# Performance work log

Measured on AMD Instinct MI355X. Metric: run time of the kernel, lower is better.

Reference implementation:

```python
import jax, jax.numpy as jnp
import numpy as np

N_NODES = 50000
N_EDGES = 800000
IN_F = 128
HID_F = 128
OUT_F = 128
BATCH = 2


def setup_inputs() -> dict:
    key = jax.random.key(0)
    ks = jax.random.split(key, 12)
    inputs = jax.random.normal(ks[0], (BATCH, N_NODES, IN_F), dtype=jnp.float32)
    src = jax.random.randint(ks[1], (N_EDGES,), 0, N_NODES, dtype=jnp.int32)
    dst = jax.random.randint(ks[2], (N_EDGES,), 0, N_NODES, dtype=jnp.int32)
    s = 0.05
    return {
        "inputs": inputs, "src": src, "dst": dst,
        "W_self1": jax.random.normal(ks[3], (HID_F, IN_F), jnp.float32) * s,
        "W_neigh1": jax.random.normal(ks[4], (HID_F, IN_F), jnp.float32) * s,
        "b1": jnp.zeros((HID_F,), jnp.float32),
        "W_self2": jax.random.normal(ks[5], (HID_F, HID_F), jnp.float32) * s,
        "W_neigh2": jax.random.normal(ks[6], (HID_F, HID_F), jnp.float32) * s,
        "b2": jnp.zeros((HID_F,), jnp.float32),
        "W_self3": jax.random.normal(ks[7], (OUT_F, HID_F), jnp.float32) * s,
        "W_neigh3": jax.random.normal(ks[8], (OUT_F, HID_F), jnp.float32) * s,
        "b3": jnp.zeros((OUT_F,), jnp.float32),
    }


def _sage_layer(h, src, dst, deg_inv, W_self, W_neigh, b):
    # h: [N, d]; mean-aggregate over in-neighbors (src -> dst)
    msg = h[src]                                              # [E, d] gather
    agg = jax.ops.segment_sum(msg, dst, num_segments=N_NODES)  # [N, d]
    agg = agg * deg_inv[:, None]                               # mean (0 for deg-0 nodes, DGL convention)
    out = h @ W_self.T + agg @ W_neigh.T + b
    # SAGEConv activation=ReLU; outer F.relu after conv1/conv2 is idempotent
    return jax.nn.relu(out)


def reference(inputs, src, dst, W_self1, W_neigh1, b1, W_self2, W_neigh2, b2, W_self3, W_neigh3, b3):
    deg = jax.ops.segment_sum(jnp.ones((N_EDGES,), jnp.float32), dst, num_segments=N_NODES)
    deg_inv = jnp.where(deg > 0, 1.0 / jnp.maximum(deg, 1.0), 0.0)

    def per_graph(x):  # x: [N, in_feats]
        h = _sage_layer(x, src, dst, deg_inv, W_self1, W_neigh1, b1)
        h = _sage_layer(h, src, dst, deg_inv, W_self2, W_neigh2, b2)
        h = _sage_layer(h, src, dst, deg_inv, W_self3, W_neigh3, b3)
        return h

    return jax.vmap(per_graph)(inputs)  # [B, N, out_feats]
```

## Files before the change

### kernel.cpp

```cpp
#include <hip/hip_runtime.h>

#define NN 50000
#define NE 800000
#define F  128
#define NB 2
#define M2 (NB * NN)

typedef __attribute__((ext_vector_type(8))) short     bf16x8;
typedef __attribute__((ext_vector_type(4))) float     f32x4;
typedef __attribute__((ext_vector_type(8))) unsigned short u16x8;
typedef __attribute__((ext_vector_type(4))) unsigned short u16x4;

__device__ inline unsigned short f2bf_rn(float f) {
    unsigned u = __float_as_uint(f);
    u += 0x7FFFu + ((u >> 16) & 1u);
    return (unsigned short)(u >> 16);
}
__device__ inline float bf2f(unsigned short h) {
    return __uint_as_float(((unsigned)h) << 16);
}


__global__ void count_kernel(const int* __restrict__ dst, int* __restrict__ cnt) {
    int e = blockIdx.x * blockDim.x + threadIdx.x;
    if (e < NE) atomicAdd(&cnt[dst[e]], 1);
}

__global__ __launch_bounds__(1024) void scan1_kernel(const int* __restrict__ cnt,
                                                     int* __restrict__ local_ex,
                                                     int* __restrict__ blocksums) {
    __shared__ int sd[1024];
    int i = blockIdx.x * 1024 + threadIdx.x;
    int v = (i < NN) ? cnt[i] : 0;
    sd[threadIdx.x] = v;
    __syncthreads();
    for (int off = 1; off < 1024; off <<= 1) {
        int t = 0;
        if ((int)threadIdx.x >= off) t = sd[threadIdx.x - off];
        __syncthreads();
        sd[threadIdx.x] += t;
        __syncthreads();
    }
    if (i < NN) local_ex[i] = sd[threadIdx.x] - v;
    if (threadIdx.x == 1023) blocksums[blockIdx.x] = sd[1023];
}

__global__ void scan2_kernel(int* __restrict__ bs, int nb) {
    int lane = threadIdx.x;
    int v = (lane < nb) ? bs[lane] : 0;
    for (int off = 1; off < 64; off <<= 1) {
        int t = __shfl_up(v, off);
        if (lane >= off) v += t;
    }
    int ex = __shfl_up(v, 1);
    if (lane == 0) ex = 0;
    if (lane < nb) bs[lane] = ex;
}

__global__ void scan3_kernel(const int* __restrict__ local_ex, const int* __restrict__ bs,
                             const int* __restrict__ cnt,
                             int* __restrict__ rowptr, float* __restrict__ dinv) {
    int i = blockIdx.x * blockDim.x + threadIdx.x;
    if (i < NN) {
        rowptr[i] = local_ex[i] + bs[i >> 10];
        int d = cnt[i];
        dinv[i] = (d > 0) ? 1.0f / (float)d : 0.0f;
    }
    if (i == 0) rowptr[NN] = NE;
}

__global__ void fill_kernel(const int* __restrict__ src, const int* __restrict__ dst,
                            const int* __restrict__ rowptr, int* __restrict__ cursor,
                            unsigned short* __restrict__ eidx) {
    int e = blockIdx.x * blockDim.x + threadIdx.x;
    if (e < NE) {
        int d = dst[e];
        int p = rowptr[d] + atomicAdd(&cursor[d], 1);
        eidx[p] = (unsigned short)src[e];
    }
}


__global__ void wsplit_kernel(const float* __restrict__ Ws0, const float* __restrict__ Wn0,
                              const float* __restrict__ Ws1, const float* __restrict__ Wn1,
                              const float* __restrict__ Ws2, const float* __restrict__ Wn2,
                              unsigned short* __restrict__ hi, unsigned short* __restrict__ lo) {
    int idx = blockIdx.x * blockDim.x + threadIdx.x;
    int l = idx >> 15;
    int r = idx & 32767;
    int j = r >> 8, k = r & 255;
    const float* Ws = (l == 0) ? Ws0 : (l == 1) ? Ws1 : Ws2;
    const float* Wn = (l == 0) ? Wn0 : (l == 1) ? Wn1 : Wn2;
    float v = (k < 128) ? Ws[j * 128 + k] : Wn[j * 128 + (k - 128)];
    unsigned short h = f2bf_rn(v);
    hi[idx] = h;
    lo[idx] = f2bf_rn(v - bf2f(h));
}


__global__ void xsplit_kernel(const float* __restrict__ x,
                              unsigned short* __restrict__ hi, unsigned short* __restrict__ lo) {
    size_t idx = (size_t)blockIdx.x * blockDim.x + threadIdx.x;
    float4 v = *reinterpret_cast<const float4*>(&x[idx * 4]);
    int f4 = (int)(idx & 31);
    size_t row = idx >> 5;
    int b = (row >= NN) ? 1 : 0;
    size_t n = row - (size_t)b * NN;
    size_t o = ((n << 1) + b) * F + f4 * 4;
    u16x4 h4, l4;
    float vv[4] = {v.x, v.y, v.z, v.w};
#pragma unroll
    for (int i = 0; i < 4; ++i) {
        unsigned short h = f2bf_rn(vv[i]);
        h4[i] = h;
        l4[i] = f2bf_rn(vv[i] - bf2f(h));
    }
    *reinterpret_cast<u16x4*>(&hi[o]) = h4;
    *reinterpret_cast<u16x4*>(&lo[o]) = l4;
}


__global__ void aggregate_bf16(const unsigned short* __restrict__ h,
                               const int* __restrict__ rowptr, const unsigned short* __restrict__ eidx,
                               const float* __restrict__ dinv,
                               unsigned short* __restrict__ agg_hi, unsigned short* __restrict__ agg_lo) {
    int gtid = blockIdx.x * blockDim.x + threadIdx.x;
    int node = gtid >> 6;
    int lane = gtid & 63;
    if (node >= NN) return;
    int g = lane >> 5, li = lane & 31;
    int s0 = rowptr[node], s1 = rowptr[node + 1];

    float acc[8] = {0.f, 0.f, 0.f, 0.f, 0.f, 0.f, 0.f, 0.f};

    for (int e = s0; e < s1; e += 8) {
        int sidx[4];
        u16x8 vv[4];
#pragma unroll
        for (int j = 0; j < 4; ++j) {
            int ee = e + 2 * j + g;
            sidx[j] = (ee < s1) ? (int)eidx[ee] : -1;
        }
#pragma unroll
        for (int j = 0; j < 4; ++j)
            if (sidx[j] >= 0)
                vv[j] = *reinterpret_cast<const u16x8*>(&h[(size_t)sidx[j] * 256 + li * 8]);
#pragma unroll
        for (int j = 0; j < 4; ++j)
            if (sidx[j] >= 0) {
#pragma unroll
                for (int i = 0; i < 8; ++i) acc[i] += bf2f(vv[j][i]);
            }
    }

#pragma unroll
    for (int i = 0; i < 8; ++i) acc[i] += __shfl_xor(acc[i], 32);

    if (g == 0) {
        float di = dinv[node];
        u16x8 h8, l8;
#pragma unroll
        for (int i = 0; i < 8; ++i) {
            float v = acc[i] * di;
            unsigned short hh = f2bf_rn(v);
            h8[i] = hh;
            l8[i] = f2bf_rn(v - bf2f(hh));
        }
        *reinterpret_cast<u16x8*>(&agg_hi[(size_t)node * 256 + li * 8]) = h8;
        *reinterpret_cast<u16x8*>(&agg_lo[(size_t)node * 256 + li * 8]) = l8;
    }
}


__global__ __launch_bounds__(256) void sage_gemm_mfma(
    const unsigned short* __restrict__ Shi, const unsigned short* __restrict__ Slo,
    const unsigned short* __restrict__ Ghi, const unsigned short* __restrict__ Glo,
    const unsigned short* __restrict__ Whi, const unsigned short* __restrict__ Wlo,
    const float* __restrict__ bias,
    float* __restrict__ outf, unsigned short* __restrict__ ohi, unsigned short* __restrict__ olo,
    int final_layer)
{
    __shared__ unsigned short lds[2][4][4096];

    int tid = threadIdx.x;
    int lane = tid & 63, wave = tid >> 6;
    int wm = wave >> 1, wn = wave & 1;
    int l15 = lane & 15, kg = lane >> 4;
    int row_base = blockIdx.x * 128;
    if (row_base > M2 - 128) row_base = M2 - 128;

    int s_sub = lane >> 2;
    int s_g   = lane & 3;

    auto stage = [&](int buf, int ks) {
        const unsigned short* Ah = (ks < 4) ? Shi : Ghi;
        const unsigned short* Al = (ks < 4) ? Slo : Glo;
        int ka = (ks & 3) * 32;
        int kb = ks * 32;
#pragma unroll
        for (int jj = 0; jj < 2; ++jj) {
            int j = wave * 2 + jj;
            int r = j * 16 + s_sub;
            int kgs = s_g ^ ((r >> 1) & 3);
            const unsigned short* pah = &Ah[(size_t)(row_base + r) * F + ka + kgs * 8];
            const unsigned short* pal = &Al[(size_t)(row_base + r) * F + ka + kgs * 8];
            const unsigned short* pwh = &Whi[(size_t)r * 256 + kb + kgs * 8];
            const unsigned short* pwl = &Wlo[(size_t)r * 256 + kb + kgs * 8];
            __builtin_amdgcn_global_load_lds((const __attribute__((address_space(1))) void*)pah,
                (__attribute__((address_space(3))) void*)&lds[buf][0][j * 512], 16, 0, 0);
            __builtin_amdgcn_global_load_lds((const __attribute__((address_space(1))) void*)pal,
                (__attribute__((address_space(3))) void*)&lds[buf][1][j * 512], 16, 0, 0);
            __builtin_amdgcn_global_load_lds((const __attribute__((address_space(1))) void*)pwh,
                (__attribute__((address_space(3))) void*)&lds[buf][2][j * 512], 16, 0, 0);
            __builtin_amdgcn_global_load_lds((const __attribute__((address_space(1))) void*)pwl,
                (__attribute__((address_space(3))) void*)&lds[buf][3][j * 512], 16, 0, 0);
        }
    };

    f32x4 acc[4][4];
#pragma unroll
    for (int m = 0; m < 4; ++m)
#pragma unroll
        for (int n = 0; n < 4; ++n) acc[m][n] = (f32x4){0.f, 0.f, 0.f, 0.f};

    int bcol[4];
    float bv[4];
#pragma unroll
    for (int n = 0; n < 4; ++n) {
        bcol[n] = wn * 64 + n * 16 + l15;
        bv[n] = bias[bcol[n]];
    }

    stage(0, 0);
    __syncthreads();

#pragma unroll
    for (int ks = 0; ks < 8; ++ks) {
        int buf = ks & 1;
        if (ks < 7) stage(buf ^ 1, ks + 1);

        bf16x8 ah[4], al[4], bh[4], bl[4];
#pragma unroll
        for (int m = 0; m < 4; ++m) {
            int r = wm * 64 + m * 16 + l15;
            int p = (r * 4 + (kg ^ ((r >> 1) & 3))) * 8;
            ah[m] = *reinterpret_cast<const bf16x8*>(&lds[buf][0][p]);
            al[m] = *reinterpret_cast<const bf16x8*>(&lds[buf][1][p]);
        }
#pragma unroll
        for (int n = 0; n < 4; ++n) {
            int c = wn * 64 + n * 16 + l15;
            int p = (c * 4 + (kg ^ ((c >> 1) & 3))) * 8;
            bh[n] = *reinterpret_cast<const bf16x8*>(&lds[buf][2][p]);
            bl[n] = *reinterpret_cast<const bf16x8*>(&lds[buf][3][p]);
        }

#pragma unroll
        for (int m = 0; m < 4; ++m)
#pragma unroll
            for (int n = 0; n < 4; ++n) {
                acc[m][n] = __builtin_amdgcn_mfma_f32_16x16x32_bf16(ah[m], bh[n], acc[m][n], 0, 0, 0);
                acc[m][n] = __builtin_amdgcn_mfma_f32_16x16x32_bf16(ah[m], bl[n], acc[m][n], 0, 0, 0);
                acc[m][n] = __builtin_amdgcn_mfma_f32_16x16x32_bf16(al[m], bh[n], acc[m][n], 0, 0, 0);
            }

        __syncthreads();
    }

    int wrow = row_base + wm * 64;
#pragma unroll
    for (int m = 0; m < 4; ++m) {
#pragma unroll
        for (int i = 0; i < 4; ++i) {
            int r = wrow + m * 16 + kg * 4 + i;
            if (r < M2) {
#pragma unroll
                for (int n = 0; n < 4; ++n) {
                    float v = fmaxf(acc[m][n][i] + bv[n], 0.f);
                    if (final_layer) {
                        size_t off = ((size_t)(r & 1) * NN + (size_t)(r >> 1)) * F + bcol[n];
                        outf[off] = v;
                    } else {
                        size_t off = (size_t)r * F + bcol[n];
                        unsigned short hh = f2bf_rn(v);
                        ohi[off] = hh;
                        olo[off] = f2bf_rn(v - bf2f(hh));
                    }
                }
            }
        }
    }
}


extern "C" void kernel_launch(void* const* d_in, const int* in_sizes, int n_in,
                              void* d_out, int out_size, void* d_ws, size_t ws_size,
                              hipStream_t stream) {
    const float* x  = (const float*)d_in[0];
    const int* src  = (const int*)d_in[1];
    const int* dst  = (const int*)d_in[2];
    const float* Wp[3][2] = {
        {(const float*)d_in[3], (const float*)d_in[4]},
        {(const float*)d_in[6], (const float*)d_in[7]},
        {(const float*)d_in[9], (const float*)d_in[10]},
    };
    const float* bp[3] = {(const float*)d_in[5], (const float*)d_in[8], (const float*)d_in[11]};
    float* out = (float*)d_out;

    char* p = (char*)d_ws;
    auto alloc = [&](size_t b) -> void* {
        void* r = (void*)p;
        p += (b + 255) & ~(size_t)255;
        return r;
    };
    int* cnt      = (int*)alloc(sizeof(int) * NN);
    int* cursor   = (int*)alloc(sizeof(int) * NN);
    int* rowptr   = (int*)alloc(sizeof(int) * (NN + 1));
    int* local_ex = (int*)alloc(sizeof(int) * NN);
    int* bsums    = (int*)alloc(sizeof(int) * 64);
    unsigned short* eidx = (unsigned short*)alloc(sizeof(short) * NE);
    float* dinv   = (float*)alloc(sizeof(float) * NN);
    unsigned short* Whi = (unsigned short*)alloc(sizeof(short) * 3 * 128 * 256);
    unsigned short* Wlo = (unsigned short*)alloc(sizeof(short) * 3 * 128 * 256);
    unsigned short* Xhi = (unsigned short*)alloc(sizeof(short) * M2 * F);
    unsigned short* Xlo = (unsigned short*)alloc(sizeof(short) * M2 * F);
    unsigned short* Yhi = (unsigned short*)alloc(sizeof(short) * M2 * F);
    unsigned short* Ylo = (unsigned short*)alloc(sizeof(short) * M2 * F);
    unsigned short* Ghi = (unsigned short*)alloc(sizeof(short) * M2 * F);
    unsigned short* Glo = (unsigned short*)alloc(sizeof(short) * M2 * F);

    hipMemsetAsync(cnt, 0, (char*)rowptr - (char*)cnt, stream);

    count_kernel<<<(NE + 255) / 256, 256, 0, stream>>>(dst, cnt);
    const int NSB = (NN + 1023) / 1024;
    scan1_kernel<<<NSB, 1024, 0, stream>>>(cnt, local_ex, bsums);
    scan2_kernel<<<1, 64, 0, stream>>>(bsums, NSB);
    scan3_kernel<<<(NN + 255) / 256, 256, 0, stream>>>(local_ex, bsums, cnt, rowptr, dinv);
    fill_kernel<<<(NE + 255) / 256, 256, 0, stream>>>(src, dst, rowptr, cursor, eidx);

    wsplit_kernel<<<3 * 128, 256, 0, stream>>>(Wp[0][0], Wp[0][1], Wp[1][0], Wp[1][1],
                                               Wp[2][0], Wp[2][1], Whi, Wlo);

    xsplit_kernel<<<((size_t)NB * NN * F / 4) / 256, 256, 0, stream>>>(x, Xhi, Xlo);

    const int AGG_BLOCKS  = (NN * 64) / 256;
    const int GEMM_BLOCKS = (M2 + 127) / 128;

    aggregate_bf16<<<AGG_BLOCKS, 256, 0, stream>>>(Xhi, rowptr, eidx, dinv, Ghi, Glo);
    sage_gemm_mfma<<<GEMM_BLOCKS, 256, 0, stream>>>(Xhi, Xlo, Ghi, Glo,
                                                    Whi + 0 * 32768, Wlo + 0 * 32768, bp[0],
                                                    nullptr, Yhi, Ylo, 0);
    aggregate_bf16<<<AGG_BLOCKS, 256, 0, stream>>>(Yhi, rowptr, eidx, dinv, Ghi, Glo);
    sage_gemm_mfma<<<GEMM_BLOCKS, 256, 0, stream>>>(Yhi, Ylo, Ghi, Glo,
                                                    Whi + 1 * 32768, Wlo + 1 * 32768, bp[1],
                                                    nullptr, Xhi, Xlo, 0);
    aggregate_bf16<<<AGG_BLOCKS, 256, 0, stream>>>(Xhi, rowptr, eidx, dinv, Ghi, Glo);
    sage_gemm_mfma<<<GEMM_BLOCKS, 256, 0, stream>>>(Xhi, Xlo, Ghi, Glo,
                                                    Whi + 2 * 32768, Wlo + 2 * 32768, bp[2],
                                                    out, nullptr, nullptr, 1);
}
```

Before: 395.0 us.

## Drop low-order bf16 split for aggregates and hidden activations

Stores the aggregated neighbour features and the hidden-layer activations as a single bf16 value instead of a hi/lo bf16 pair. The input layer still uses the lo correction for the self term, selected through a template parameter. This removes the lo buffers' writes and gathers and cuts the MFMA count per k-step on most steps, lowering memory traffic in both the aggregation and the GEMM kernels. In exchange, the hidden activations and aggregates carry only bf16 precision, which may strain the accuracy tolerance.

```diff
diff --git a/kernel.cpp b/kernel.cpp
--- a/kernel.cpp
+++ b/kernel.cpp
@@ -123,7 +123,7 @@
 __global__ void aggregate_bf16(const unsigned short* __restrict__ h,
                                const int* __restrict__ rowptr, const unsigned short* __restrict__ eidx,
                                const float* __restrict__ dinv,
-                               unsigned short* __restrict__ agg_hi, unsigned short* __restrict__ agg_lo) {
+                               unsigned short* __restrict__ agg_hi) {
     int gtid = blockIdx.x * blockDim.x + threadIdx.x;
     int node = gtid >> 6;
     int lane = gtid & 63;
@@ -158,29 +158,24 @@
 
     if (g == 0) {
         float di = dinv[node];
-        u16x8 h8, l8;
-#pragma unroll
-        for (int i = 0; i < 8; ++i) {
-            float v = acc[i] * di;
-            unsigned short hh = f2bf_rn(v);
-            h8[i] = hh;
-            l8[i] = f2bf_rn(v - bf2f(hh));
-        }
+        u16x8 h8;
+#pragma unroll
+        for (int i = 0; i < 8; ++i) h8[i] = f2bf_rn(acc[i] * di);
         *reinterpret_cast<u16x8*>(&agg_hi[(size_t)node * 256 + li * 8]) = h8;
-        *reinterpret_cast<u16x8*>(&agg_lo[(size_t)node * 256 + li * 8]) = l8;
-    }
-}
-
-
+    }
+}
+
+
+template<int SELF_LO>
 __global__ __launch_bounds__(256) void sage_gemm_mfma(
     const unsigned short* __restrict__ Shi, const unsigned short* __restrict__ Slo,
-    const unsigned short* __restrict__ Ghi, const unsigned short* __restrict__ Glo,
+    const unsigned short* __restrict__ Ghi,
     const unsigned short* __restrict__ Whi, const unsigned short* __restrict__ Wlo,
     const float* __restrict__ bias,
-    float* __restrict__ outf, unsigned short* __restrict__ ohi, unsigned short* __restrict__ olo,
+    float* __restrict__ outf, unsigned short* __restrict__ ohi,
     int final_layer)
 {
-    __shared__ unsigned short lds[2][4][4096];
+    __shared__ unsigned short lds[2][3 + SELF_LO][4096];
 
     int tid = threadIdx.x;
     int lane = tid & 63, wave = tid >> 6;
@@ -194,7 +189,6 @@
 
     auto stage = [&](int buf, int ks) {
         const unsigned short* Ah = (ks < 4) ? Shi : Ghi;
-        const unsigned short* Al = (ks < 4) ? Slo : Glo;
         int ka = (ks & 3) * 32;
         int kb = ks * 32;
 #pragma unroll
@@ -203,17 +197,19 @@
             int r = j * 16 + s_sub;
             int kgs = s_g ^ ((r >> 1) & 3);
             const unsigned short* pah = &Ah[(size_t)(row_base + r) * F + ka + kgs * 8];
-            const unsigned short* pal = &Al[(size_t)(row_base + r) * F + ka + kgs * 8];
             const unsigned short* pwh = &Whi[(size_t)r * 256 + kb + kgs * 8];
             const unsigned short* pwl = &Wlo[(size_t)r * 256 + kb + kgs * 8];
             __builtin_amdgcn_global_load_lds((const __attribute__((address_space(1))) void*)pah,
                 (__attribute__((address_space(3))) void*)&lds[buf][0][j * 512], 16, 0, 0);
-            __builtin_amdgcn_global_load_lds((const __attribute__((address_space(1))) void*)pal,
+            __builtin_amdgcn_global_load_lds((const __attribute__((address_space(1))) void*)pwh,
                 (__attribute__((address_space(3))) void*)&lds[buf][1][j * 512], 16, 0, 0);
-            __builtin_amdgcn_global_load_lds((const __attribute__((address_space(1))) void*)pwh,
+            __builtin_amdgcn_global_load_lds((const __attribute__((address_space(1))) void*)pwl,
                 (__attribute__((address_space(3))) void*)&lds[buf][2][j * 512], 16, 0, 0);
-            __builtin_amdgcn_global_load_lds((const __attribute__((address_space(1))) void*)pwl,
-                (__attribute__((address_space(3))) void*)&lds[buf][3][j * 512], 16, 0, 0);
+            if (SELF_LO && ks < 4) {
+                const unsigned short* pal = &Slo[(size_t)(row_base + r) * F + ka + kgs * 8];
+                __builtin_amdgcn_global_load_lds((const __attribute__((address_space(1))) void*)pal,
+                    (__attribute__((address_space(3))) void*)&lds[buf][3][j * 512], 16, 0, 0);
+            }
         }
     };
 
@@ -245,14 +241,15 @@
             int r = wm * 64 + m * 16 + l15;
             int p = (r * 4 + (kg ^ ((r >> 1) & 3))) * 8;
             ah[m] = *reinterpret_cast<const bf16x8*>(&lds[buf][0][p]);
-            al[m] = *reinterpret_cast<const bf16x8*>(&lds[buf][1][p]);
+            if (SELF_LO && ks < 4)
+                al[m] = *reinterpret_cast<const bf16x8*>(&lds[buf][3][p]);
         }
 #pragma unroll
         for (int n = 0; n < 4; ++n) {
             int c = wn * 64 + n * 16 + l15;
             int p = (c * 4 + (kg ^ ((c >> 1) & 3))) * 8;
-            bh[n] = *reinterpret_cast<const bf16x8*>(&lds[buf][2][p]);
-            bl[n] = *reinterpret_cast<const bf16x8*>(&lds[buf][3][p]);
+            bh[n] = *reinterpret_cast<const bf16x8*>(&lds[buf][1][p]);
+            bl[n] = *reinterpret_cast<const bf16x8*>(&lds[buf][2][p]);
         }
 
 #pragma unroll
@@ -261,7 +258,8 @@
             for (int n = 0; n < 4; ++n) {
                 acc[m][n] = __builtin_amdgcn_mfma_f32_16x16x32_bf16(ah[m], bh[n], acc[m][n], 0, 0, 0);
                 acc[m][n] = __builtin_amdgcn_mfma_f32_16x16x32_bf16(ah[m], bl[n], acc[m][n], 0, 0, 0);
-                acc[m][n] = __builtin_amdgcn_mfma_f32_16x16x32_bf16(al[m], bh[n], acc[m][n], 0, 0, 0);
+                if (SELF_LO && ks < 4)
+                    acc[m][n] = __builtin_amdgcn_mfma_f32_16x16x32_bf16(al[m], bh[n], acc[m][n], 0, 0, 0);
             }
 
         __syncthreads();
@@ -282,9 +280,7 @@
                         outf[off] = v;
                     } else {
                         size_t off = (size_t)r * F + bcol[n];
-                        unsigned short hh = f2bf_rn(v);
-                        ohi[off] = hh;
-                        olo[off] = f2bf_rn(v - bf2f(hh));
+                        ohi[off] = f2bf_rn(v);
                     }
                 }
             }
@@ -322,12 +318,11 @@
     float* dinv   = (float*)alloc(sizeof(float) * NN);
     unsigned short* Whi = (unsigned short*)alloc(sizeof(short) * 3 * 128 * 256);
     unsigned short* Wlo = (unsigned short*)alloc(sizeof(short) * 3 * 128 * 256);
-    unsigned short* Xhi = (unsigned short*)alloc(sizeof(short) * M2 * F);
-    unsigned short* Xlo = (unsigned short*)alloc(sizeof(short) * M2 * F);
-    unsigned short* Yhi = (unsigned short*)alloc(sizeof(short) * M2 * F);
-    unsigned short* Ylo = (unsigned short*)alloc(sizeof(short) * M2 * F);
-    unsigned short* Ghi = (unsigned short*)alloc(sizeof(short) * M2 * F);
-    unsigned short* Glo = (unsigned short*)alloc(sizeof(short) * M2 * F);
+    unsigned short* X0hi = (unsigned short*)alloc(sizeof(short) * M2 * F);
+    unsigned short* X0lo = (unsigned short*)alloc(sizeof(short) * M2 * F);
+    unsigned short* H1   = (unsigned short*)alloc(sizeof(short) * M2 * F);
+    unsigned short* H2   = (unsigned short*)alloc(sizeof(short) * M2 * F);
+    unsigned short* Ghi  = (unsigned short*)alloc(sizeof(short) * M2 * F);
 
     hipMemsetAsync(cnt, 0, (char*)rowptr - (char*)cnt, stream);
 
@@ -341,21 +336,21 @@
     wsplit_kernel<<<3 * 128, 256, 0, stream>>>(Wp[0][0], Wp[0][1], Wp[1][0], Wp[1][1],
                                                Wp[2][0], Wp[2][1], Whi, Wlo);
 
-    xsplit_kernel<<<((size_t)NB * NN * F / 4) / 256, 256, 0, stream>>>(x, Xhi, Xlo);
+    xsplit_kernel<<<((size_t)NB * NN * F / 4) / 256, 256, 0, stream>>>(x, X0hi, X0lo);
 
     const int AGG_BLOCKS  = (NN * 64) / 256;
     const int GEMM_BLOCKS = (M2 + 127) / 128;
 
-    aggregate_bf16<<<AGG_BLOCKS, 256, 0, stream>>>(Xhi, rowptr, eidx, dinv, Ghi, Glo);
-    sage_gemm_mfma<<<GEMM_BLOCKS, 256, 0, stream>>>(Xhi, Xlo, Ghi, Glo,
-                                                    Whi + 0 * 32768, Wlo + 0 * 32768, bp[0],
-                                                    nullptr, Yhi, Ylo, 0);
-    aggregate_bf16<<<AGG_BLOCKS, 256, 0, stream>>>(Yhi, rowptr, eidx, dinv, Ghi, Glo);
-    sage_gemm_mfma<<<GEMM_BLOCKS, 256, 0, stream>>>(Yhi, Ylo, Ghi, Glo,
-                                                    Whi + 1 * 32768, Wlo + 1 * 32768, bp[1],
-                                                    nullptr, Xhi, Xlo, 0);
-    aggregate_bf16<<<AGG_BLOCKS, 256, 0, stream>>>(Xhi, rowptr, eidx, dinv, Ghi, Glo);
-    sage_gemm_mfma<<<GEMM_BLOCKS, 256, 0, stream>>>(Xhi, Xlo, Ghi, Glo,
-                                                    Whi + 2 * 32768, Wlo + 2 * 32768, bp[2],
-                                                    out, nullptr, nullptr, 1);
-}
+    aggregate_bf16<<<AGG_BLOCKS, 256, 0, stream>>>(X0hi, rowptr, eidx, dinv, Ghi);
+    sage_gemm_mfma<1><<<GEMM_BLOCKS, 256, 0, stream>>>(X0hi, X0lo, Ghi,
+                                                       Whi + 0 * 32768, Wlo + 0 * 32768, bp[0],
+                                                       nullptr, H1, 0);
+    aggregate_bf16<<<AGG_BLOCKS, 256, 0, stream>>>(H1, rowptr, eidx, dinv, Ghi);
+    sage_gemm_mfma<0><<<GEMM_BLOCKS, 256, 0, stream>>>(H1, nullptr, Ghi,
+                                                       Whi + 1 * 32768, Wlo + 1 * 32768, bp[1],
+                                                       nullptr, H2, 0);
+    aggregate_bf16<<<AGG_BLOCKS, 256, 0, stream>>>(H2, rowptr, eidx, dinv, Ghi);
+    sage_gemm_mfma<0><<<GEMM_BLOCKS, 256, 0, stream>>>(H2, nullptr, Ghi,
+                                                       Whi + 2 * 32768, Wlo + 2 * 32768, bp[2],
+                                                       out, nullptr, 1);
+}
```

Result: faster. 352.3 us (median of 2 runs) (-10.8%).
